# Optimization experiments

Hardware: AMD Instinct MI355X
Metric: run time of the kernel (lower is better)

Reference implementation:

```python
import jax, jax.numpy as jnp
import numpy as np

NPOINT = 1024
RADIUS = 0.4
NSAMPLE = 32
BN_EPS = 1e-3  # keras BatchNormalization default epsilon


def _fps(xyz, npoint):
    # xyz: [N,3] -> indices [npoint] via farthest point sampling (seed index 0)
    N = xyz.shape[0]

    def step(carry, _):
        dists, far = carry
        d = jnp.sum((xyz - xyz[far]) ** 2, axis=-1)
        dists = jnp.minimum(dists, d)
        return (dists, jnp.argmax(dists).astype(jnp.int32)), far

    init = (jnp.full((N,), 1e10, dtype=xyz.dtype), jnp.asarray(0, dtype=jnp.int32))
    _, idx = jax.lax.scan(step, init, None, length=npoint)
    return idx


def _ball_query(xyz, new_xyz, radius, nsample):
    # xyz: [N,3], new_xyz: [S,3] -> idx [S,nsample]
    # First up-to-nsample points (in original index order) within radius of each
    # center; slots past the count are filled with the first found index
    # (matching the CUDA query_ball_point semantics).
    N = xyz.shape[0]
    d2 = jnp.sum((new_xyz[:, None, :] - xyz[None, :, :]) ** 2, axis=-1)  # [S,N]
    key = jnp.where(d2 < radius * radius, jnp.arange(N, dtype=jnp.int32), N)
    sk = jnp.sort(key, axis=-1)[:, :nsample]          # first valid indices, padded with N
    first = sk[:, :1]
    first = jnp.where(first < N, first, 0)            # fallback if no neighbor found
    idx = jnp.where(sk < N, sk, first)
    return idx.astype(jnp.int32)


def _gather(pts, idx):
    # pts: [B,N,C], idx: [B,...] -> [B,...,C]
    return jax.vmap(lambda p, i: p[i])(pts, idx)


def _conv_bn_relu(x, W, b, g, be):
    # 1x1 conv over [B,P,S,Cin] + batchnorm (training mode, batch stats) + relu
    y = jnp.einsum('bpsc,co->bpso', x, W) + b
    m = jnp.mean(y, axis=(0, 1, 2))
    v = jnp.var(y, axis=(0, 1, 2))
    y = (y - m) * jax.lax.rsqrt(v + BN_EPS) * g + be
    return jax.nn.relu(y)


def setup_inputs() -> dict:
    key = jax.random.key(0)
    ks = jax.random.split(key, 8)
    B, N, C = 16, 4096, 64
    xyz = jax.random.normal(ks[0], (B, N, 3), dtype=jnp.float32)
    points = jax.random.normal(ks[1], (B, N, C), dtype=jnp.float32)
    chans = [3 + C, 64, 64, 128]
    inp = {'xyz': xyz, 'points': points}
    for i in range(3):
        cin, cout = chans[i], chans[i + 1]
        limit = np.sqrt(6.0 / (cin + cout))  # glorot uniform
        inp[f'W{i}'] = jax.random.uniform(ks[2 + i], (cin, cout), jnp.float32, -limit, limit)
        inp[f'b{i}'] = jnp.zeros((cout,), jnp.float32)
        inp[f'g{i}'] = jnp.ones((cout,), jnp.float32)
        inp[f'be{i}'] = jnp.zeros((cout,), jnp.float32)
    return inp


def reference(xyz, points, W0, b0, g0, be0, W1, b1, g1, be1, W2, b2, g2, be2):
    xyz_c = jax.lax.stop_gradient(xyz)
    fps_idx = jax.vmap(lambda p: _fps(p, NPOINT))(xyz_c)           # [B,NPOINT]
    new_xyz = _gather(xyz, fps_idx)                                 # [B,NPOINT,3]
    idx = jax.vmap(lambda p, c: _ball_query(p, c, RADIUS, NSAMPLE))(
        xyz_c, jax.lax.stop_gradient(new_xyz))                      # [B,NPOINT,NSAMPLE]
    grouped_xyz = _gather(xyz, idx) - new_xyz[:, :, None, :]        # centered local coords
    grouped_points = _gather(points, idx)                           # [B,NPOINT,NSAMPLE,C]
    new_points = jnp.concatenate([grouped_xyz, grouped_points], axis=-1)
    new_points = _conv_bn_relu(new_points, W0, b0, g0, be0)
    new_points = _conv_bn_relu(new_points, W1, b1, g1, be1)
    new_points = _conv_bn_relu(new_points, W2, b2, g2, be2)
    new_points = jnp.max(new_points, axis=2)                        # max-pool over nsample
    return (new_xyz, new_points, idx)
```

## Files before the change

kernel.cpp:

```cpp
#include <hip/hip_runtime.h>

static constexpr int NB      = 16;
static constexpr int NPTS    = 4096;
static constexpr int NPOINTS = 1024;
static constexpr int NSAMP   = 32;
static constexpr int CIN0    = 67;
static constexpr int C0      = 64;
static constexpr int C1      = 64;
static constexpr int C2      = 128;
static constexpr size_t MROWS = (size_t)NB * NPOINTS * NSAMP;
#define RAD2 0.16f
#define BN_EPS 0.001f

__device__ __forceinline__ float4 uld4(const float* __restrict__ p) {
    return *(const float4* __restrict__)p;
}

__device__ __forceinline__ unsigned short f2bf(float f) {
    const unsigned u = __float_as_uint(f);
    return (unsigned short)((u + 0x7fffu + ((u >> 16) & 1u)) >> 16);
}
__device__ __forceinline__ float bf2f(unsigned short h) {
    return __uint_as_float((unsigned)h << 16);
}

template<int CTRL>
__device__ __forceinline__ float dppf(float v) {
    return __int_as_float(__builtin_amdgcn_update_dpp(0, __float_as_int(v),
                                                      CTRL, 0xF, 0xF, false));
}
template<int CTRL>
__device__ __forceinline__ float dpps(float v) {
    return __int_as_float(__builtin_amdgcn_update_dpp(__float_as_int(v), __float_as_int(v),
                                                      CTRL, 0xF, 0xF, false));
}
__device__ __forceinline__ float dpp_sum64(float v) {
    v += dppf<0x111>(v); v += dppf<0x112>(v); v += dppf<0x114>(v); v += dppf<0x118>(v);
    v += dppf<0x142>(v); v += dppf<0x143>(v);
    return v;
}
__device__ __forceinline__ float dpp_psum8(float v) {
    v += dppf<0x111>(v); v += dppf<0x112>(v); v += dppf<0x114>(v);
    return v;
}
__device__ __forceinline__ float dpp_psum16(float v) {
    v += dppf<0x111>(v); v += dppf<0x112>(v); v += dppf<0x114>(v); v += dppf<0x118>(v);
    return v;
}
__device__ __forceinline__ float dpp_max32(float v) {
    v = fmaxf(v, dpps<0x111>(v)); v = fmaxf(v, dpps<0x112>(v));
    v = fmaxf(v, dpps<0x114>(v)); v = fmaxf(v, dpps<0x118>(v));
    v = fmaxf(v, dpps<0x142>(v));
    return v;
}
__device__ __forceinline__ float dpp_min32(float v) {
    v = fminf(v, dpps<0x111>(v)); v = fminf(v, dpps<0x112>(v));
    v = fminf(v, dpps<0x114>(v)); v = fminf(v, dpps<0x118>(v));
    v = fminf(v, dpps<0x142>(v));
    return v;
}
template<int CTRL>
__device__ __forceinline__ void kstep(unsigned long long& k) {
    const unsigned hi = (unsigned)(k >> 32);
    const unsigned lo = (unsigned)(k & 0xffffffffull);
    const unsigned ohi = (unsigned)__builtin_amdgcn_update_dpp((int)hi, (int)hi, CTRL, 0xF, 0xF, false);
    const unsigned olo = (unsigned)__builtin_amdgcn_update_dpp((int)lo, (int)lo, CTRL, 0xF, 0xF, false);
    const unsigned long long ok = ((unsigned long long)ohi << 32) | olo;
    if (ok > k) k = ok;
}

__global__ __launch_bounds__(512) void fps_kernel(const float* __restrict__ xyz,
                                                  float* __restrict__ out_newxyz,
                                                  float* __restrict__ wsz,
                                                  const float* __restrict__ points,
                                                  const float* __restrict__ W0,
                                                  float* __restrict__ P)
{
    if (blockIdx.x == NB) {
        for (int i = threadIdx.x; i < 1024; i += 512) wsz[i] = 0.f;
        return;
    }
    if (blockIdx.x > NB) {
        const int r = (blockIdx.x - NB - 1) * 512 + threadIdx.x;
        const float4* pr = (const float4*)(points + (size_t)r * 64);
        float x[64];
#pragma unroll
        for (int j = 0; j < 16; ++j) {
            const float4 v = pr[j];
            x[4*j+0] = v.x; x[4*j+1] = v.y; x[4*j+2] = v.z; x[4*j+3] = v.w;
        }
        float acc[64];
#pragma unroll
        for (int o = 0; o < 64; ++o) acc[o] = 0.f;
#pragma unroll 2
        for (int k = 0; k < 64; ++k) {
            const float xk = x[k];
#pragma unroll
            for (int oc = 0; oc < 16; ++oc) {
                const float4 w4 = uld4(W0 + (3 + k) * 64 + 4 * oc);
                acc[4*oc+0] = fmaf(xk, w4.x, acc[4*oc+0]);
                acc[4*oc+1] = fmaf(xk, w4.y, acc[4*oc+1]);
                acc[4*oc+2] = fmaf(xk, w4.z, acc[4*oc+2]);
                acc[4*oc+3] = fmaf(xk, w4.w, acc[4*oc+3]);
            }
        }
        float4* po = (float4*)(P + (size_t)r * 64);
#pragma unroll
        for (int oc = 0; oc < 16; ++oc)
            po[oc] = make_float4(acc[4*oc+0], acc[4*oc+1], acc[4*oc+2], acc[4*oc+3]);
        return;
    }

    __shared__ float sx[NPTS], sy[NPTS], sz[NPTS];
    __shared__ int   sidx[NPOINTS];
    __shared__ __align__(16) unsigned long long redk[2][8];

    const int b    = blockIdx.x;
    const int tid  = threadIdx.x;
    const int lane = tid & 63;
    const int wv   = tid >> 6;

    const float* base = xyz + (size_t)b * NPTS * 3;
    for (int i = tid; i < NPTS; i += 512) {
        sx[i] = base[i * 3 + 0];
        sy[i] = base[i * 3 + 1];
        sz[i] = base[i * 3 + 2];
    }
    __syncthreads();

    float px[8], py[8], pz[8], dd[8];
#pragma unroll
    for (int j = 0; j < 8; ++j) {
        const int i = tid + j * 512;
        px[j] = sx[i]; py[j] = sy[i]; pz[j] = sz[i];
        dd[j] = 1e10f;
    }

    int   far = 0;
    float fx = sx[0], fy = sy[0], fz = sz[0];
#pragma unroll 1
    for (int it = 0; it < NPOINTS; ++it) {
        if (tid == 0) sidx[it] = far;
        float bv = -1.0f; int bi = 0;
#pragma unroll
        for (int j = 0; j < 8; ++j) {
            const float dx = __fsub_rn(px[j], fx);
            const float dy = __fsub_rn(py[j], fy);
            const float dz = __fsub_rn(pz[j], fz);
            const float d  = __fadd_rn(__fadd_rn(__fmul_rn(dx, dx), __fmul_rn(dy, dy)),
                                       __fmul_rn(dz, dz));
            dd[j] = fminf(dd[j], d);
            if (dd[j] > bv) { bv = dd[j]; bi = tid + j * 512; }
        }
        unsigned long long k = ((unsigned long long)__float_as_uint(bv) << 32)
                             | (unsigned)(4095 - bi);
        kstep<0x111>(k);
        kstep<0x112>(k);
        kstep<0x114>(k);
        kstep<0x118>(k);
        kstep<0x142>(k);
        kstep<0x143>(k);

        const int pb = it & 1;
        if (lane == 63) redk[pb][wv] = k;
        __syncthreads();
        unsigned long long ck = redk[pb][0];
#pragma unroll
        for (int w = 1; w < 8; ++w) {
            const unsigned long long ok = redk[pb][w];
            if (ok > ck) ck = ok;
        }
        const int ci = 4095 - (int)(unsigned)(ck & 0xffffffffull);
        far = ci;
        fx = sx[ci]; fy = sy[ci]; fz = sz[ci];
    }
    __syncthreads();
    for (int it = tid; it < NPOINTS; it += 512) {
        const int ii = sidx[it];
        float* o = out_newxyz + ((size_t)b * NPOINTS + it) * 3;
        o[0] = sx[ii]; o[1] = sy[ii]; o[2] = sz[ii];
    }
}

__global__ __launch_bounds__(256) void ball_kernel(const float* __restrict__ xyz,
                                                   const float* __restrict__ newxyz,
                                                   float* __restrict__ out_idx_f)
{
    __shared__ int sel[4][NSAMP];
    const int tid  = threadIdx.x;
    const int lane = tid & 63;
    const int widx = tid >> 6;
    const int w = blockIdx.x * 4 + widx;
    const int b = w >> 10;

    const float cx = newxyz[(size_t)w * 3 + 0];
    const float cy = newxyz[(size_t)w * 3 + 1];
    const float cz = newxyz[(size_t)w * 3 + 2];
    const float* base = xyz + (size_t)b * NPTS * 3;

    int total = 0;
    for (int c = 0; c < NPTS / 64 && total < NSAMP; ++c) {
        const int n = c * 64 + lane;
        const float dx = __fsub_rn(cx, base[n * 3 + 0]);
        const float dy = __fsub_rn(cy, base[n * 3 + 1]);
        const float dz = __fsub_rn(cz, base[n * 3 + 2]);
        const float d2 = __fadd_rn(__fadd_rn(__fmul_rn(dx, dx), __fmul_rn(dy, dy)),
                                   __fmul_rn(dz, dz));
        const bool pred = d2 < RAD2;
        const unsigned long long mask = __ballot(pred);
        if (pred) {
            const int pos = total + (int)__popcll(mask & ((1ull << lane) - 1ull));
            if (pos < NSAMP) sel[widx][pos] = n;
        }
        total += (int)__popcll(mask);
    }
    __syncthreads();
    if (lane < NSAMP) {
        const int first = sel[widx][0];
        const int v = (lane < total) ? sel[widx][lane] : first;
        out_idx_f[(size_t)w * NSAMP + lane] = (float)v;
    }
}

__device__ __forceinline__ void stats4q8(float a0, float a1, float a2, float a3,
                                         float2* sa, bool wr)
{
    float q0 = a0*a0, q1 = a1*a1, q2 = a2*a2, q3 = a3*a3;
    a0 = dpp_psum8(a0); q0 = dpp_psum8(q0);
    a1 = dpp_psum8(a1); q1 = dpp_psum8(q1);
    a2 = dpp_psum8(a2); q2 = dpp_psum8(q2);
    a3 = dpp_psum8(a3); q3 = dpp_psum8(q3);
    if (wr) {
        *(float4*)&sa[0] = make_float4(a0, q0, a1, q1);
        *(float4*)&sa[2] = make_float4(a2, q2, a3, q3);
    }
}

__device__ __forceinline__ void stats4(float a0, float a1, float a2, float a3,
                                       float* sa, int lane)
{
    float q0 = a0*a0, q1 = a1*a1, q2 = a2*a2, q3 = a3*a3;
    a0 = dpp_sum64(a0); q0 = dpp_sum64(q0);
    a1 = dpp_sum64(a1); q1 = dpp_sum64(q1);
    a2 = dpp_sum64(a2); q2 = dpp_sum64(q2);
    a3 = dpp_sum64(a3); q3 = dpp_sum64(q3);
    if (lane == 63) {
        sa[0] += a0; sa[1] += q0; sa[2] += a1; sa[3] += q1;
        sa[4] += a2; sa[5] += q2; sa[6] += a3; sa[7] += q3;
    }
}

__global__ __launch_bounds__(256) void preP_kernel(const float* __restrict__ points,
                                                   const float* __restrict__ W0,
                                                   float* __restrict__ P)
{
    const int r = blockIdx.x * 256 + threadIdx.x;
    const float4* pr = (const float4*)(points + (size_t)r * 64);
    float x[64];
#pragma unroll
    for (int j = 0; j < 16; ++j) {
        const float4 v = pr[j];
        x[4*j+0] = v.x; x[4*j+1] = v.y; x[4*j+2] = v.z; x[4*j+3] = v.w;
    }
    float acc[64];
#pragma unroll
    for (int o = 0; o < 64; ++o) acc[o] = 0.f;
#pragma unroll 2
    for (int k = 0; k < 64; ++k) {
        const float xk = x[k];
#pragma unroll
        for (int oc = 0; oc < 16; ++oc) {
            const float4 w4 = uld4(W0 + (3 + k) * 64 + 4 * oc);
            acc[4*oc+0] = fmaf(xk, w4.x, acc[4*oc+0]);
            acc[4*oc+1] = fmaf(xk, w4.y, acc[4*oc+1]);
            acc[4*oc+2] = fmaf(xk, w4.z, acc[4*oc+2]);
            acc[4*oc+3] = fmaf(xk, w4.w, acc[4*oc+3]);
        }
    }
    float4* po = (float4*)(P + (size_t)r * 64);
#pragma unroll
    for (int oc = 0; oc < 16; ++oc)
        po[oc] = make_float4(acc[4*oc+0], acc[4*oc+1], acc[4*oc+2], acc[4*oc+3]);
}

__device__ __forceinline__ void layer0_dedup(
    const float* __restrict__ xyz, const float* __restrict__ P,
    const float* __restrict__ newxyz, const float* __restrict__ idxf,
    const float* __restrict__ W0, const float* __restrict__ b0,
    int r, float* x1)
{
    const int i  = (int)idxf[r];
    const int bb = r >> 15;
    const int pp = (r >> 5) & 1023;
    const float* pz = xyz + ((size_t)bb * NPTS + i) * 3;
    const float* nz = newxyz + ((size_t)bb * NPOINTS + pp) * 3;
    const float r0 = pz[0] - nz[0];
    const float r1 = pz[1] - nz[1];
    const float r2 = pz[2] - nz[2];
    const float4* prow = (const float4*)(P + ((size_t)bb * NPTS + i) * 64);
#pragma unroll
    for (int oc = 0; oc < 16; ++oc) {
        const float4 pv = prow[oc];
        const float4 bv = uld4(b0 + 4 * oc);
        const float4 wa = uld4(W0 + 0 * 64 + 4 * oc);
        const float4 wb = uld4(W0 + 1 * 64 + 4 * oc);
        const float4 wc = uld4(W0 + 2 * 64 + 4 * oc);
        x1[4*oc+0] = fmaf(r0, wa.x, fmaf(r1, wb.x, fmaf(r2, wc.x, bv.x + pv.x)));
        x1[4*oc+1] = fmaf(r0, wa.y, fmaf(r1, wb.y, fmaf(r2, wc.y, bv.y + pv.y)));
        x1[4*oc+2] = fmaf(r0, wa.z, fmaf(r1, wb.z, fmaf(r2, wc.z, bv.z + pv.z)));
        x1[4*oc+3] = fmaf(r0, wa.w, fmaf(r1, wb.w, fmaf(r2, wc.w, bv.w + pv.w)));
    }
}

template<int C>
__device__ __forceinline__ void bn_inline(const float* __restrict__ gs,
                                          const float* __restrict__ g,
                                          const float* __restrict__ be,
                                          float* ssl, int tid)
{
    if (tid < C) {
        const float inv  = 1.0f / (float)MROWS;
        const float mean = gs[2*tid] * inv;
        const float var  = fmaxf(0.f, gs[2*tid+1] * inv - mean * mean);
        const float sc   = g[tid] / sqrtf(var + BN_EPS);
        ssl[tid]     = sc;
        ssl[C + tid] = fmaf(-mean, sc, be[tid]);
    }
}

__global__ __launch_bounds__(256, 4) void pass0_kernel(
    const float* __restrict__ xyz, const float* __restrict__ P,
    const float* __restrict__ newxyz, const float* __restrict__ idxf,
    const float* __restrict__ W0, const float* __restrict__ b0,
    float* __restrict__ gstats)
{
    __shared__ float2 sacc[32][C0 + 1];
    const int tid  = threadIdx.x;
    const int lane = tid & 63;
    const int wv   = tid >> 6;
    const int slot = wv * 8 + (lane >> 3);
    const bool wr  = (lane & 7) == 7;

    const int r = blockIdx.x * 256 + tid;
    float x1[C0];
    layer0_dedup(xyz, P, newxyz, idxf, W0, b0, r, x1);

#pragma unroll
    for (int oc = 0; oc < 16; ++oc)
        stats4q8(x1[4*oc+0], x1[4*oc+1], x1[4*oc+2], x1[4*oc+3], &sacc[slot][4*oc], wr);

    __syncthreads();
    for (int j = tid; j < C0; j += 256) {
        float s = 0.f, q = 0.f;
#pragma unroll
        for (int v = 0; v < 32; ++v) { s += sacc[v][j].x; q += sacc[v][j].y; }
        atomicAdd(&gstats[2*j], s);
        atomicAdd(&gstats[2*j+1], q);
    }
}

__global__ __launch_bounds__(256, 3) void pass1Y_kernel(
    const float* __restrict__ xyz, const float* __restrict__ P,
    const float* __restrict__ newxyz, const float* __restrict__ idxf,
    const float* __restrict__ W0, const float* __restrict__ b0,
    const float* __restrict__ W1, const float* __restrict__ b1,
    const float* __restrict__ gs0, const float* __restrict__ g0,
    const float* __restrict__ be0,
    float* __restrict__ gstats, unsigned short* __restrict__ y1b)
{
    __shared__ float2 sacc[32][C0 + 1];
    __shared__ float ssl[2 * C0];
    const int tid  = threadIdx.x;
    const int lane = tid & 63;
    const int wv   = tid >> 6;
    const int slot = wv * 8 + (lane >> 3);
    const bool wr  = (lane & 7) == 7;

    bn_inline<C0>(gs0, g0, be0, ssl, tid);
    __syncthreads();

    const int r = blockIdx.x * 256 + tid;
    float x1[C0];
    layer0_dedup(xyz, P, newxyz, idxf, W0, b0, r, x1);
#pragma unroll
    for (int o = 0; o < C0; ++o)
        x1[o] = fmaxf(0.f, fmaf(x1[o], ssl[o], ssl[64 + o]));

    float y1[C1];
#pragma unroll
    for (int o = 0; o < C1; o += 4) {
        const float4 bv = uld4(b1 + o);
        y1[o] = bv.x; y1[o+1] = bv.y; y1[o+2] = bv.z; y1[o+3] = bv.w;
    }
#pragma unroll 2
    for (int k = 0; k < C0; ++k) {
        const float xk = x1[k];
#pragma unroll
        for (int oc = 0; oc < 16; ++oc) {
            const float4 w4 = uld4(W1 + k * 64 + 4 * oc);
            y1[4*oc+0] = fmaf(xk, w4.x, y1[4*oc+0]);
            y1[4*oc+1] = fmaf(xk, w4.y, y1[4*oc+1]);
            y1[4*oc+2] = fmaf(xk, w4.z, y1[4*oc+2]);
            y1[4*oc+3] = fmaf(xk, w4.w, y1[4*oc+3]);
        }
    }

#pragma unroll
    for (int oc = 0; oc < 16; ++oc)
        stats4q8(y1[4*oc+0], y1[4*oc+1], y1[4*oc+2], y1[4*oc+3], &sacc[slot][4*oc], wr);

    uint4* yo = (uint4*)(y1b + (size_t)r * 64);
#pragma unroll
    for (int gq = 0; gq < 8; ++gq) {
        union { unsigned short u[8]; uint4 v; } pk;
#pragma unroll
        for (int e = 0; e < 8; ++e) pk.u[e] = f2bf(y1[8*gq+e]);
        yo[gq] = pk.v;
    }

    __syncthreads();
    for (int j = tid; j < C0; j += 256) {
        float s = 0.f, q = 0.f;
#pragma unroll
        for (int v = 0; v < 32; ++v) { s += sacc[v][j].x; q += sacc[v][j].y; }
        atomicAdd(&gstats[2*j], s);
        atomicAdd(&gstats[2*j+1], q);
    }
}

__global__ __launch_bounds__(256, 3) void p2Y_kernel(
    const unsigned short* __restrict__ y1b,
    const float* __restrict__ W2, const float* __restrict__ b2,
    const float* __restrict__ gs1, const float* __restrict__ g1,
    const float* __restrict__ be1,
    float* __restrict__ gstats, float2* __restrict__ mnmx)
{
    __shared__ float2 sacc[32][C2 + 1];
    __shared__ float ssl[2 * C1];
    const int tid  = threadIdx.x;
    const int lane = tid & 63;
    const int wv   = tid >> 6;
    const int slot = wv * 8 + (lane >> 3);
    const bool wr  = (lane & 7) == 7;

    bn_inline<C1>(gs1, g1, be1, ssl, tid);
    __syncthreads();

    const int r = blockIdx.x * 256 + tid;

    float y1[C1];
    {
        const uint4* yi = (const uint4*)(y1b + (size_t)r * 64);
#pragma unroll
        for (int gq = 0; gq < 8; ++gq) {
            union { uint4 v; unsigned short u[8]; } pk;
            pk.v = yi[gq];
#pragma unroll
            for (int e = 0; e < 8; ++e)
                y1[8*gq+e] = bf2f(pk.u[e]);
        }
    }
#pragma unroll
    for (int o = 0; o < C1; ++o)
        y1[o] = fmaxf(0.f, fmaf(y1[o], ssl[o], ssl[64 + o]));

    const int gbase = blockIdx.x * 8 + 2 * wv;
    float2* mb = mnmx + ((size_t)gbase + (lane >> 5)) * C2;

#pragma unroll 1
    for (int to = 0; to < 2; ++to) {
        const int ob = to * 64;
        float a2[64];
#pragma unroll
        for (int o = 0; o < 64; o += 4) {
            const float4 bv = uld4(b2 + ob + o);
            a2[o] = bv.x; a2[o+1] = bv.y; a2[o+2] = bv.z; a2[o+3] = bv.w;
        }
#pragma unroll 2
        for (int k = 0; k < C1; ++k) {
            const float xk = y1[k];
#pragma unroll
            for (int o = 0; o < 64; o += 4) {
                const float4 w4 = uld4(W2 + k * C2 + ob + o);
                a2[o+0] = fmaf(xk, w4.x, a2[o+0]);
                a2[o+1] = fmaf(xk, w4.y, a2[o+1]);
                a2[o+2] = fmaf(xk, w4.z, a2[o+2]);
                a2[o+3] = fmaf(xk, w4.w, a2[o+3]);
            }
        }

#pragma unroll
        for (int o = 0; o < 64; ++o) {
            const float v = a2[o];
            const float s  = dpp_psum8(v);
            const float q  = dpp_psum8(v * v);
            const float mn = dpp_min32(v);
            const float mx = dpp_max32(v);
            if (wr) sacc[slot][ob + o] = make_float2(s, q);
            if (lane == 31 || lane == 63) mb[ob + o] = make_float2(mn, mx);
        }
    }

    __syncthreads();
    for (int j = tid; j < C2; j += 256) {
        float s = 0.f, q = 0.f;
#pragma unroll
        for (int v = 0; v < 32; ++v) { s += sacc[v][j].x; q += sacc[v][j].y; }
        atomicAdd(&gstats[2*j], s);
        atomicAdd(&gstats[2*j+1], q);
    }
}

__global__ __launch_bounds__(256) void finY_kernel(const float2* __restrict__ mnmx,
                                                   const float* __restrict__ gs2,
                                                   const float* __restrict__ g2,
                                                   const float* __restrict__ be2,
                                                   float* __restrict__ out_np)
{
    const int t = blockIdx.x * 256 + threadIdx.x;
    const int g = t >> 7;
    const int o = t & 127;
    const float inv  = 1.0f / (float)MROWS;
    const float mean = gs2[2*o] * inv;
    const float var  = fmaxf(0.f, gs2[2*o+1] * inv - mean * mean);
    const float sc   = g2[o] / sqrtf(var + BN_EPS);
    const float sh   = fmaf(-mean, sc, be2[o]);
    const float2 mm  = mnmx[(size_t)g * C2 + o];
    const float y    = (sc >= 0.f) ? mm.y : mm.x;
    out_np[t] = fmaxf(0.f, fmaf(y, sc, sh));
}

template<int C>
__global__ void ss_kernel(const float* __restrict__ gs, const float* __restrict__ g,
                          const float* __restrict__ be, float* __restrict__ ss)
{
    const int o = threadIdx.x;
    const float inv  = 1.0f / (float)MROWS;
    const float mean = gs[2*o] * inv;
    const float var  = fmaxf(0.f, gs[2*o+1] * inv - mean * mean);
    const float sc   = g[o] / sqrtf(var + BN_EPS);
    ss[o]     = sc;
    ss[C + o] = fmaf(-mean, sc, be[o]);
}

template<int PHASE>
__global__ __launch_bounds__(256, 2) void passP_kernel(
    const float* __restrict__ xyz, const float* __restrict__ P,
    const float* __restrict__ newxyz, const float* __restrict__ idxf,
    const float* __restrict__ W0, const float* __restrict__ b0,
    const float* __restrict__ W1, const float* __restrict__ b1,
    const float* __restrict__ W2, const float* __restrict__ b2,
    const float* __restrict__ ss0, const float* __restrict__ ss1,
    const float* __restrict__ ss2,
    float* __restrict__ gstats, float* __restrict__ out_np)
{
    constexpr int CS = (PHASE == 2) ? C2 : C0;
    __shared__ float sacc[4][2 * CS];

    const int tid  = threadIdx.x;
    const int lane = tid & 63;
    const int wv   = tid >> 6;

    if constexpr (PHASE <= 2) {
        for (int j = tid; j < 8 * CS; j += 256) (&sacc[0][0])[j] = 0.f;
        __syncthreads();
    }

    const int r = blockIdx.x * 256 + tid;
    float x1[C0];
    layer0_dedup(xyz, P, newxyz, idxf, W0, b0, r, x1);

    if constexpr (PHASE == 0) {
#pragma unroll
        for (int oc = 0; oc < 16; ++oc)
            stats4(x1[4*oc+0], x1[4*oc+1], x1[4*oc+2], x1[4*oc+3], &sacc[wv][8*oc], lane);
    } else {
#pragma unroll
        for (int o = 0; o < C0; ++o)
            x1[o] = fmaxf(0.f, fmaf(x1[o], ss0[o], ss0[64 + o]));

        float y1[C1];
#pragma unroll
        for (int o = 0; o < C1; o += 4) {
            const float4 bv = uld4(b1 + o);
            y1[o] = bv.x; y1[o+1] = bv.y; y1[o+2] = bv.z; y1[o+3] = bv.w;
        }
#pragma unroll 2
        for (int k = 0; k < C0; ++k) {
            const float xk = x1[k];
#pragma unroll
            for (int oc = 0; oc < 16; ++oc) {
                const float4 w4 = uld4(W1 + k * 64 + 4 * oc);
                y1[4*oc+0] = fmaf(xk, w4.x, y1[4*oc+0]);
                y1[4*oc+1] = fmaf(xk, w4.y, y1[4*oc+1]);
                y1[4*oc+2] = fmaf(xk, w4.z, y1[4*oc+2]);
                y1[4*oc+3] = fmaf(xk, w4.w, y1[4*oc+3]);
            }
        }

        if constexpr (PHASE == 1) {
#pragma unroll
            for (int oc = 0; oc < 16; ++oc)
                stats4(y1[4*oc+0], y1[4*oc+1], y1[4*oc+2], y1[4*oc+3], &sacc[wv][8*oc], lane);
        } else {
#pragma unroll
            for (int o = 0; o < C1; ++o)
                y1[o] = fmaxf(0.f, fmaf(y1[o], ss1[o], ss1[64 + o]));

            float a2[C2];
#pragma unroll
            for (int o = 0; o < C2; o += 4) {
                const float4 bv = uld4(b2 + o);
                a2[o] = bv.x; a2[o+1] = bv.y; a2[o+2] = bv.z; a2[o+3] = bv.w;
            }
#pragma unroll 2
            for (int k = 0; k < C1; ++k) {
                const float xk = y1[k];
#pragma unroll
                for (int o = 0; o < C2; o += 4) {
                    const float4 w4 = uld4(W2 + k * C2 + o);
                    a2[o+0] = fmaf(xk, w4.x, a2[o+0]);
                    a2[o+1] = fmaf(xk, w4.y, a2[o+1]);
                    a2[o+2] = fmaf(xk, w4.z, a2[o+2]);
                    a2[o+3] = fmaf(xk, w4.w, a2[o+3]);
                }
            }

            if constexpr (PHASE == 2) {
#pragma unroll
                for (int o = 0; o < C2; ++o) {
                    const float s = dpp_sum64(a2[o]);
                    const float q = dpp_sum64(a2[o] * a2[o]);
                    if (lane == 63) { sacc[wv][2*o] += s; sacc[wv][2*o+1] += q; }
                }
            } else {
                const int g = r >> 5;
#pragma unroll
                for (int o = 0; o < C2; ++o) {
                    float v = fmaxf(0.f, fmaf(a2[o], ss2[o], ss2[C2 + o]));
                    v = dpp_max32(v);
                    if (lane == 31 || lane == 63) out_np[(size_t)g * C2 + o] = v;
                }
            }
        }
    }

    if constexpr (PHASE <= 2) {
        __syncthreads();
        for (int j = tid; j < 2 * CS; j += 256)
            atomicAdd(&gstats[j], sacc[0][j] + sacc[1][j] + sacc[2][j] + sacc[3][j]);
    }
}

template<int PHASE>
__global__ __launch_bounds__(128) void pass_kernel(
    const float* __restrict__ xyz, const float* __restrict__ points,
    const float* __restrict__ newxyz, const float* __restrict__ idxf,
    const float* __restrict__ W0, const float* __restrict__ b0,
    const float* __restrict__ W1, const float* __restrict__ b1,
    const float* __restrict__ W2, const float* __restrict__ b2,
    const float* __restrict__ ss0, const float* __restrict__ ss1,
    const float* __restrict__ ss2,
    float* __restrict__ gstats, float* __restrict__ out_np)
{
    constexpr int CS = (PHASE == 2) ? C2 : C0;
    __shared__ float xld[(PHASE >= 1) ? (64 * 128) : 1];
    __shared__ float sacc[2][2 * CS];

    const int tid  = threadIdx.x;
    const int lane = tid & 63;
    const int wv   = tid >> 6;

    if constexpr (PHASE <= 2) {
        for (int j = tid; j < 2 * 2 * CS; j += 128) (&sacc[0][0])[j] = 0.f;
        __syncthreads();
    }

    const int r  = blockIdx.x * 128 + tid;
    const int i  = (int)idxf[r];
    const int bb = r >> 15;
    const int pp = (r >> 5) & 1023;

    float x[CIN0];
    {
        const float* pz = xyz + ((size_t)bb * NPTS + i) * 3;
        const float* nz = newxyz + ((size_t)bb * NPOINTS + pp) * 3;
        x[0] = pz[0] - nz[0];
        x[1] = pz[1] - nz[1];
        x[2] = pz[2] - nz[2];
        const float4* p4 = (const float4*)(points + ((size_t)bb * NPTS + i) * 64);
#pragma unroll
        for (int j = 0; j < 16; ++j) {
            const float4 v = p4[j];
            x[3+4*j+0] = v.x; x[3+4*j+1] = v.y; x[3+4*j+2] = v.z; x[3+4*j+3] = v.w;
        }
    }

#pragma unroll 1
    for (int oc = 0; oc < 16; ++oc) {
        const float4 bv = uld4(b0 + 4*oc);
        float a0 = bv.x, a1 = bv.y, a2 = bv.z, a3 = bv.w;
#pragma unroll
        for (int k = 0; k < CIN0; ++k) {
            const float4 w4 = uld4(W0 + k*64 + 4*oc);
            a0 = fmaf(x[k], w4.x, a0); a1 = fmaf(x[k], w4.y, a1);
            a2 = fmaf(x[k], w4.z, a2); a3 = fmaf(x[k], w4.w, a3);
        }
        if constexpr (PHASE == 0) {
            stats4(a0, a1, a2, a3, &sacc[wv][8*oc], lane);
        } else {
            xld[(4*oc+0)*128 + tid] = fmaxf(0.f, fmaf(a0, ss0[4*oc+0], ss0[64+4*oc+0]));
            xld[(4*oc+1)*128 + tid] = fmaxf(0.f, fmaf(a1, ss0[4*oc+1], ss0[64+4*oc+1]));
            xld[(4*oc+2)*128 + tid] = fmaxf(0.f, fmaf(a2, ss0[4*oc+2], ss0[64+4*oc+2]));
            xld[(4*oc+3)*128 + tid] = fmaxf(0.f, fmaf(a3, ss0[4*oc+3], ss0[64+4*oc+3]));
        }
    }

    if constexpr (PHASE == 1) {
#pragma unroll 1
        for (int oc = 0; oc < 16; ++oc) {
            const float4 bv = uld4(b1 + 4*oc);
            float a0 = bv.x, a1 = bv.y, a2 = bv.z, a3 = bv.w;
#pragma unroll
            for (int k = 0; k < 64; ++k) {
                const float xk = xld[k*128 + tid];
                const float4 w4 = uld4(W1 + k*64 + 4*oc);
                a0 = fmaf(xk, w4.x, a0); a1 = fmaf(xk, w4.y, a1);
                a2 = fmaf(xk, w4.z, a2); a3 = fmaf(xk, w4.w, a3);
            }
            stats4(a0, a1, a2, a3, &sacc[wv][8*oc], lane);
        }
    }

    if constexpr (PHASE >= 2) {
        float acc2[C2];
#pragma unroll
        for (int o = 0; o < C2; o += 4) {
            const float4 bv = uld4(b2 + o);
            acc2[o] = bv.x; acc2[o+1] = bv.y; acc2[o+2] = bv.z; acc2[o+3] = bv.w;
        }
#pragma unroll 1
        for (int oc = 0; oc < 16; ++oc) {
            const float4 bv = uld4(b1 + 4*oc);
            float a0 = bv.x, a1 = bv.y, a2 = bv.z, a3 = bv.w;
#pragma unroll
            for (int k = 0; k < 64; ++k) {
                const float xk = xld[k*128 + tid];
                const float4 w4 = uld4(W1 + k*64 + 4*oc);
                a0 = fmaf(xk, w4.x, a0); a1 = fmaf(xk, w4.y, a1);
                a2 = fmaf(xk, w4.z, a2); a3 = fmaf(xk, w4.w, a3);
            }
            const float xc0 = fmaxf(0.f, fmaf(a0, ss1[4*oc+0], ss1[64+4*oc+0]));
            const float xc1 = fmaxf(0.f, fmaf(a1, ss1[4*oc+1], ss1[64+4*oc+1]));
            const float xc2 = fmaxf(0.f, fmaf(a2, ss1[4*oc+2], ss1[64+4*oc+2]));
            const float xc3 = fmaxf(0.f, fmaf(a3, ss1[4*oc+3], ss1[64+4*oc+3]));
#pragma unroll
            for (int o = 0; o < C2; o += 4) {
                const float4 wA = uld4(W2 + (4*oc+0)*C2 + o);
                const float4 wB = uld4(W2 + (4*oc+1)*C2 + o);
                const float4 wC = uld4(W2 + (4*oc+2)*C2 + o);
                const float4 wD = uld4(W2 + (4*oc+3)*C2 + o);
                acc2[o+0] = fmaf(xc0, wA.x, fmaf(xc1, wB.x, fmaf(xc2, wC.x, fmaf(xc3, wD.x, acc2[o+0]))));
                acc2[o+1] = fmaf(xc0, wA.y, fmaf(xc1, wB.y, fmaf(xc2, wC.y, fmaf(xc3, wD.y, acc2[o+1]))));
                acc2[o+2] = fmaf(xc0, wA.z, fmaf(xc1, wB.z, fmaf(xc2, wC.z, fmaf(xc3, wD.z, acc2[o+2]))));
                acc2[o+3] = fmaf(xc0, wA.w, fmaf(xc1, wB.w, fmaf(xc2, wC.w, fmaf(xc3, wD.w, acc2[o+3]))));
            }
        }

        if constexpr (PHASE == 2) {
#pragma unroll
            for (int o = 0; o < C2; ++o) {
                const float s = dpp_sum64(acc2[o]);
                const float q = dpp_sum64(acc2[o] * acc2[o]);
                if (lane == 63) { sacc[wv][2*o] += s; sacc[wv][2*o+1] += q; }
            }
        } else {
            const int g = r >> 5;
#pragma unroll
            for (int o = 0; o < C2; ++o) {
                float v = fmaxf(0.f, fmaf(acc2[o], ss2[o], ss2[C2+o]));
                v = dpp_max32(v);
                if (lane == 31 || lane == 63) out_np[(size_t)g * C2 + o] = v;
            }
        }
    }

    if constexpr (PHASE <= 2) {
        __syncthreads();
        for (int j = tid; j < 2 * CS; j += 128)
            atomicAdd(&gstats[j], sacc[0][j] + sacc[1][j]);
    }
}

extern "C" void kernel_launch(void* const* d_in, const int* in_sizes, int n_in,
                              void* d_out, int out_size, void* d_ws, size_t ws_size,
                              hipStream_t stream)
{
    (void)in_sizes; (void)n_in; (void)out_size;
    const float* xyz    = (const float*)d_in[0];
    const float* points = (const float*)d_in[1];
    const float* W0  = (const float*)d_in[2];
    const float* b0  = (const float*)d_in[3];
    const float* g0  = (const float*)d_in[4];
    const float* be0 = (const float*)d_in[5];
    const float* W1  = (const float*)d_in[6];
    const float* b1  = (const float*)d_in[7];
    const float* g1  = (const float*)d_in[8];
    const float* be1 = (const float*)d_in[9];
    const float* W2  = (const float*)d_in[10];
    const float* b2  = (const float*)d_in[11];
    const float* g2  = (const float*)d_in[12];
    const float* be2 = (const float*)d_in[13];

    float* out = (float*)d_out;
    float* out_newxyz = out;
    float* out_newpts = out + (size_t)NB * NPOINTS * 3;
    float* out_idx    = out_newpts + (size_t)NB * NPOINTS * C2;

    float* wsf = (float*)d_ws;
    float* gs0 = wsf + 0;
    float* gs1 = wsf + 128;
    float* gs2 = wsf + 256;
    float* ss0 = wsf + 512;
    float* ss1 = wsf + 640;
    float* ss2 = wsf + 768;
    const size_t PBYTES  = (size_t)NB * NPTS * C0 * 4;
    const size_t MMBYTES = (size_t)NB * NPOINTS * 2 * C2 * 4;
    const size_t YBYTES  = MROWS * C1 * 2;
    float* P    = (float*)((char*)d_ws + 65536);
    float* mnmx = (float*)((char*)d_ws + 65536 + PBYTES);
    unsigned short* y1b = (unsigned short*)((char*)d_ws + 65536 + PBYTES + MMBYTES);

    const bool haveP  = ws_size >= (65536 + PBYTES);
    const bool haveMM = ws_size >= (65536 + PBYTES + MMBYTES);
    const bool haveY  = ws_size >= (65536 + PBYTES + MMBYTES + YBYTES);

    const int frontGrid = NB + 1 + (haveP ? (NB * NPTS / 512) : 0);
    fps_kernel<<<frontGrid, 512, 0, stream>>>(xyz, out_newxyz, wsf, points, W0, P);
    ball_kernel<<<(NB * NPOINTS) / 4, 256, 0, stream>>>(xyz, out_newxyz, out_idx);

    if (haveY) {
        const int grid = (int)(MROWS / 256);
        pass0_kernel<<<grid, 256, 0, stream>>>(xyz, P, out_newxyz, out_idx,
                                               W0, b0, gs0);
        pass1Y_kernel<<<grid, 256, 0, stream>>>(xyz, P, out_newxyz, out_idx,
                                                W0, b0, W1, b1, gs0, g0, be0,
                                                gs1, y1b);
        p2Y_kernel<<<grid, 256, 0, stream>>>(y1b, W2, b2, gs1, g1, be1,
                                             gs2, (float2*)mnmx);
        finY_kernel<<<NB * NPOINTS * C2 / 256, 256, 0, stream>>>((const float2*)mnmx,
                                                                 gs2, g2, be2, out_newpts);
    } else if (haveP) {
        const int grid = (int)(MROWS / 256);
        passP_kernel<0><<<grid, 256, 0, stream>>>(xyz, P, out_newxyz, out_idx,
                                                  W0, b0, W1, b1, W2, b2,
                                                  ss0, ss1, ss2, gs0, nullptr);
        ss_kernel<C0><<<1, C0, 0, stream>>>(gs0, g0, be0, ss0);
        passP_kernel<1><<<grid, 256, 0, stream>>>(xyz, P, out_newxyz, out_idx,
                                                  W0, b0, W1, b1, W2, b2,
                                                  ss0, ss1, ss2, gs1, nullptr);
        ss_kernel<C1><<<1, C1, 0, stream>>>(gs1, g1, be1, ss1);
        passP_kernel<2><<<grid, 256, 0, stream>>>(xyz, P, out_newxyz, out_idx,
                                                  W0, b0, W1, b1, W2, b2,
                                                  ss0, ss1, ss2, gs2, nullptr);
        ss_kernel<C2><<<1, C2, 0, stream>>>(gs2, g2, be2, ss2);
        passP_kernel<3><<<grid, 256, 0, stream>>>(xyz, P, out_newxyz, out_idx,
                                                  W0, b0, W1, b1, W2, b2,
                                                  ss0, ss1, ss2, nullptr, out_newpts);
        (void)haveMM;
    } else {
        const int grid = (int)(MROWS / 128);
        pass_kernel<0><<<grid, 128, 0, stream>>>(xyz, points, out_newxyz, out_idx,
                                                 W0, b0, W1, b1, W2, b2,
                                                 ss0, ss1, ss2, gs0, nullptr);
        ss_kernel<C0><<<1, C0, 0, stream>>>(gs0, g0, be0, ss0);
        pass_kernel<1><<<grid, 128, 0, stream>>>(xyz, points, out_newxyz, out_idx,
                                                 W0, b0, W1, b1, W2, b2,
                                                 ss0, ss1, ss2, gs1, nullptr);
        ss_kernel<C1><<<1, C1, 0, stream>>>(gs1, g1, be1, ss1);
        pass_kernel<2><<<grid, 128, 0, stream>>>(xyz, points, out_newxyz, out_idx,
                                                 W0, b0, W1, b1, W2, b2,
                                                 ss0, ss1, ss2, gs2, nullptr);
        ss_kernel<C2><<<1, C2, 0, stream>>>(gs2, g2, be2, ss2);
        pass_kernel<3><<<grid, 128, 0, stream>>>(xyz, points, out_newxyz, out_idx,
                                                 W0, b0, W1, b1, W2, b2,
                                                 ss0, ss1, ss2, nullptr, out_newpts);
    }
}
```

Baseline: 1.304 ms.

## Use bf16 MFMA for layer-2 conv and hoist BN scale/shift into kernels

Replaces the per-thread FP32 FMA loop of the third 1x1 conv with 32x32x16 bf16 MFMA instructions. W2 is pre-transposed to bf16 in the front kernel, and per-group min/max plus sum/sumsq are reduced from the MFMA accumulator layout. BN scale/shift computation moves from inline per-block code into separate ss_kernel launches. Stats reduction in pass0/pass1 switches to 16-lane partial sums accumulated in zeroed shared memory. Activations are rounded to bf16 before the matmul, which lowers precision, and the change adds two small kernel launches.

```diff
diff --git a/kernel.cpp b/kernel.cpp
--- a/kernel.cpp
+++ b/kernel.cpp
@@ -24,6 +24,10 @@
     return __uint_as_float((unsigned)h << 16);
 }
 
+typedef short bf16x8 __attribute__((ext_vector_type(8)));
+typedef float f32x16 __attribute__((ext_vector_type(16)));
+union UB { uint4 u; bf16x8 h; };
+
 template<int CTRL>
 __device__ __forceinline__ float dppf(float v) {
     return __int_as_float(__builtin_amdgcn_update_dpp(0, __float_as_int(v),
@@ -37,10 +41,6 @@
 __device__ __forceinline__ float dpp_sum64(float v) {
     v += dppf<0x111>(v); v += dppf<0x112>(v); v += dppf<0x114>(v); v += dppf<0x118>(v);
     v += dppf<0x142>(v); v += dppf<0x143>(v);
-    return v;
-}
-__device__ __forceinline__ float dpp_psum8(float v) {
-    v += dppf<0x111>(v); v += dppf<0x112>(v); v += dppf<0x114>(v);
     return v;
 }
 __device__ __forceinline__ float dpp_psum16(float v) {
@@ -74,10 +74,18 @@
                                                   float* __restrict__ wsz,
                                                   const float* __restrict__ points,
                                                   const float* __restrict__ W0,
-                                                  float* __restrict__ P)
+                                                  float* __restrict__ P,
+                                                  const float* __restrict__ W2,
+                                                  unsigned short* __restrict__ W2t)
 {
     if (blockIdx.x == NB) {
         for (int i = threadIdx.x; i < 1024; i += 512) wsz[i] = 0.f;
+        if (W2t) {
+            for (int i = threadIdx.x; i < C2 * C1; i += 512) {
+                const int n = i >> 6, k = i & 63;
+                W2t[i] = f2bf(W2[(size_t)k * C2 + n]);
+            }
+        }
         return;
     }
     if (blockIdx.x > NB) {
@@ -222,17 +230,17 @@
     }
 }
 
-__device__ __forceinline__ void stats4q8(float a0, float a1, float a2, float a3,
-                                         float2* sa, bool wr)
+__device__ __forceinline__ void stats4q(float a0, float a1, float a2, float a3,
+                                        float* sa, bool wr)
 {
     float q0 = a0*a0, q1 = a1*a1, q2 = a2*a2, q3 = a3*a3;
-    a0 = dpp_psum8(a0); q0 = dpp_psum8(q0);
-    a1 = dpp_psum8(a1); q1 = dpp_psum8(q1);
-    a2 = dpp_psum8(a2); q2 = dpp_psum8(q2);
-    a3 = dpp_psum8(a3); q3 = dpp_psum8(q3);
+    a0 = dpp_psum16(a0); q0 = dpp_psum16(q0);
+    a1 = dpp_psum16(a1); q1 = dpp_psum16(q1);
+    a2 = dpp_psum16(a2); q2 = dpp_psum16(q2);
+    a3 = dpp_psum16(a3); q3 = dpp_psum16(q3);
     if (wr) {
-        *(float4*)&sa[0] = make_float4(a0, q0, a1, q1);
-        *(float4*)&sa[2] = make_float4(a2, q2, a3, q3);
+        sa[0] += a0; sa[1] += q0; sa[2] += a1; sa[3] += q1;
+        sa[4] += a2; sa[5] += q2; sa[6] += a3; sa[7] += q3;
     }
 }
 
@@ -248,39 +256,6 @@
         sa[0] += a0; sa[1] += q0; sa[2] += a1; sa[3] += q1;
         sa[4] += a2; sa[5] += q2; sa[6] += a3; sa[7] += q3;
     }
-}
-
-__global__ __launch_bounds__(256) void preP_kernel(const float* __restrict__ points,
-                                                   const float* __restrict__ W0,
-                                                   float* __restrict__ P)
-{
-    const int r = blockIdx.x * 256 + threadIdx.x;
-    const float4* pr = (const float4*)(points + (size_t)r * 64);
-    float x[64];
-#pragma unroll
-    for (int j = 0; j < 16; ++j) {
-        const float4 v = pr[j];
-        x[4*j+0] = v.x; x[4*j+1] = v.y; x[4*j+2] = v.z; x[4*j+3] = v.w;
-    }
-    float acc[64];
-#pragma unroll
-    for (int o = 0; o < 64; ++o) acc[o] = 0.f;
-#pragma unroll 2
-    for (int k = 0; k < 64; ++k) {
-        const float xk = x[k];
-#pragma unroll
-        for (int oc = 0; oc < 16; ++oc) {
-            const float4 w4 = uld4(W0 + (3 + k) * 64 + 4 * oc);
-            acc[4*oc+0] = fmaf(xk, w4.x, acc[4*oc+0]);
-            acc[4*oc+1] = fmaf(xk, w4.y, acc[4*oc+1]);
-            acc[4*oc+2] = fmaf(xk, w4.z, acc[4*oc+2]);
-            acc[4*oc+3] = fmaf(xk, w4.w, acc[4*oc+3]);
-        }
-    }
-    float4* po = (float4*)(P + (size_t)r * 64);
-#pragma unroll
-    for (int oc = 0; oc < 16; ++oc)
-        po[oc] = make_float4(acc[4*oc+0], acc[4*oc+1], acc[4*oc+2], acc[4*oc+3]);
 }
 
 __device__ __forceinline__ void layer0_dedup(
@@ -312,34 +287,21 @@
     }
 }
 
-template<int C>
-__device__ __forceinline__ void bn_inline(const float* __restrict__ gs,
-                                          const float* __restrict__ g,
-                                          const float* __restrict__ be,
-                                          float* ssl, int tid)
-{
-    if (tid < C) {
-        const float inv  = 1.0f / (float)MROWS;
-        const float mean = gs[2*tid] * inv;
-        const float var  = fmaxf(0.f, gs[2*tid+1] * inv - mean * mean);
-        const float sc   = g[tid] / sqrtf(var + BN_EPS);
-        ssl[tid]     = sc;
-        ssl[C + tid] = fmaf(-mean, sc, be[tid]);
-    }
-}
-
 __global__ __launch_bounds__(256, 4) void pass0_kernel(
     const float* __restrict__ xyz, const float* __restrict__ P,
     const float* __restrict__ newxyz, const float* __restrict__ idxf,
     const float* __restrict__ W0, const float* __restrict__ b0,
     float* __restrict__ gstats)
 {
-    __shared__ float2 sacc[32][C0 + 1];
+    __shared__ float sacc[16][2 * C0];
     const int tid  = threadIdx.x;
     const int lane = tid & 63;
     const int wv   = tid >> 6;
-    const int slot = wv * 8 + (lane >> 3);
-    const bool wr  = (lane & 7) == 7;
+    const int slot = wv * 4 + (lane >> 4);
+    const bool wr  = (lane & 15) == 15;
+
+    for (int j = tid; j < 16 * 2 * C0; j += 256) (&sacc[0][0])[j] = 0.f;
+    __syncthreads();
 
     const int r = blockIdx.x * 256 + tid;
     float x1[C0];
@@ -347,15 +309,14 @@
 
 #pragma unroll
     for (int oc = 0; oc < 16; ++oc)
-        stats4q8(x1[4*oc+0], x1[4*oc+1], x1[4*oc+2], x1[4*oc+3], &sacc[slot][4*oc], wr);
+        stats4q(x1[4*oc+0], x1[4*oc+1], x1[4*oc+2], x1[4*oc+3], &sacc[slot][8*oc], wr);
 
     __syncthreads();
-    for (int j = tid; j < C0; j += 256) {
-        float s = 0.f, q = 0.f;
-#pragma unroll
-        for (int v = 0; v < 32; ++v) { s += sacc[v][j].x; q += sacc[v][j].y; }
-        atomicAdd(&gstats[2*j], s);
-        atomicAdd(&gstats[2*j+1], q);
+    for (int j = tid; j < 2 * C0; j += 256) {
+        float s = 0.f;
+#pragma unroll
+        for (int q = 0; q < 16; ++q) s += sacc[q][j];
+        atomicAdd(&gstats[j], s);
     }
 }
 
@@ -364,19 +325,17 @@
     const float* __restrict__ newxyz, const float* __restrict__ idxf,
     const float* __restrict__ W0, const float* __restrict__ b0,
     const float* __restrict__ W1, const float* __restrict__ b1,
-    const float* __restrict__ gs0, const float* __restrict__ g0,
-    const float* __restrict__ be0,
+    const float* __restrict__ ss0,
     float* __restrict__ gstats, unsigned short* __restrict__ y1b)
 {
-    __shared__ float2 sacc[32][C0 + 1];
-    __shared__ float ssl[2 * C0];
+    __shared__ float sacc[16][2 * C0];
     const int tid  = threadIdx.x;
     const int lane = tid & 63;
     const int wv   = tid >> 6;
-    const int slot = wv * 8 + (lane >> 3);
-    const bool wr  = (lane & 7) == 7;
-
-    bn_inline<C0>(gs0, g0, be0, ssl, tid);
+    const int slot = wv * 4 + (lane >> 4);
+    const bool wr  = (lane & 15) == 15;
+
+    for (int j = tid; j < 16 * 2 * C0; j += 256) (&sacc[0][0])[j] = 0.f;
     __syncthreads();
 
     const int r = blockIdx.x * 256 + tid;
@@ -384,7 +343,7 @@
     layer0_dedup(xyz, P, newxyz, idxf, W0, b0, r, x1);
 #pragma unroll
     for (int o = 0; o < C0; ++o)
-        x1[o] = fmaxf(0.f, fmaf(x1[o], ssl[o], ssl[64 + o]));
+        x1[o] = fmaxf(0.f, fmaf(x1[o], ss0[o], ss0[64 + o]));
 
     float y1[C1];
 #pragma unroll
@@ -407,7 +366,7 @@
 
 #pragma unroll
     for (int oc = 0; oc < 16; ++oc)
-        stats4q8(y1[4*oc+0], y1[4*oc+1], y1[4*oc+2], y1[4*oc+3], &sacc[slot][4*oc], wr);
+        stats4q(y1[4*oc+0], y1[4*oc+1], y1[4*oc+2], y1[4*oc+3], &sacc[slot][8*oc], wr);
 
     uint4* yo = (uint4*)(y1b + (size_t)r * 64);
 #pragma unroll
@@ -419,95 +378,97 @@
     }
 
     __syncthreads();
-    for (int j = tid; j < C0; j += 256) {
-        float s = 0.f, q = 0.f;
-#pragma unroll
-        for (int v = 0; v < 32; ++v) { s += sacc[v][j].x; q += sacc[v][j].y; }
-        atomicAdd(&gstats[2*j], s);
-        atomicAdd(&gstats[2*j+1], q);
-    }
-}
-
-__global__ __launch_bounds__(256, 3) void p2Y_kernel(
+    for (int j = tid; j < 2 * C0; j += 256) {
+        float s = 0.f;
+#pragma unroll
+        for (int q = 0; q < 16; ++q) s += sacc[q][j];
+        atomicAdd(&gstats[j], s);
+    }
+}
+
+__global__ __launch_bounds__(256, 3) void p2Ym_kernel(
     const unsigned short* __restrict__ y1b,
-    const float* __restrict__ W2, const float* __restrict__ b2,
-    const float* __restrict__ gs1, const float* __restrict__ g1,
-    const float* __restrict__ be1,
+    const unsigned short* __restrict__ W2t,
+    const float* __restrict__ b2,
+    const float* __restrict__ ss1,
     float* __restrict__ gstats, float2* __restrict__ mnmx)
 {
-    __shared__ float2 sacc[32][C2 + 1];
-    __shared__ float ssl[2 * C1];
+    __shared__ float  ssl[2 * C1];
+    __shared__ float2 sacc[8][C2];
+    __shared__ float2 mnacc[8][C2];
+
     const int tid  = threadIdx.x;
     const int lane = tid & 63;
-    const int wv   = tid >> 6;
-    const int slot = wv * 8 + (lane >> 3);
-    const bool wr  = (lane & 7) == 7;
-
-    bn_inline<C1>(gs1, g1, be1, ssl, tid);
+    const int w    = tid >> 6;
+    const int half = lane >> 5;
+    const int col  = lane & 31;
+    const int slot = w * 2 + half;
+
+    for (int j = tid; j < 2 * C1; j += 256) ssl[j] = ss1[j];
     __syncthreads();
 
-    const int r = blockIdx.x * 256 + tid;
-
-    float y1[C1];
-    {
-        const uint4* yi = (const uint4*)(y1b + (size_t)r * 64);
-#pragma unroll
-        for (int gq = 0; gq < 8; ++gq) {
-            union { uint4 v; unsigned short u[8]; } pk;
-            pk.v = yi[gq];
-#pragma unroll
-            for (int e = 0; e < 8; ++e)
-                y1[8*gq+e] = bf2f(pk.u[e]);
-        }
-    }
-#pragma unroll
-    for (int o = 0; o < C1; ++o)
-        y1[o] = fmaxf(0.f, fmaf(y1[o], ssl[o], ssl[64 + o]));
-
-    const int gbase = blockIdx.x * 8 + 2 * wv;
-    float2* mb = mnmx + ((size_t)gbase + (lane >> 5)) * C2;
-
-#pragma unroll 1
-    for (int to = 0; to < 2; ++to) {
-        const int ob = to * 64;
-        float a2[64];
-#pragma unroll
-        for (int o = 0; o < 64; o += 4) {
-            const float4 bv = uld4(b2 + ob + o);
-            a2[o] = bv.x; a2[o+1] = bv.y; a2[o+2] = bv.z; a2[o+3] = bv.w;
-        }
-#pragma unroll 2
-        for (int k = 0; k < C1; ++k) {
-            const float xk = y1[k];
-#pragma unroll
-            for (int o = 0; o < 64; o += 4) {
-                const float4 w4 = uld4(W2 + k * C2 + ob + o);
-                a2[o+0] = fmaf(xk, w4.x, a2[o+0]);
-                a2[o+1] = fmaf(xk, w4.y, a2[o+1]);
-                a2[o+2] = fmaf(xk, w4.z, a2[o+2]);
-                a2[o+3] = fmaf(xk, w4.w, a2[o+3]);
-            }
-        }
-
-#pragma unroll
-        for (int o = 0; o < 64; ++o) {
-            const float v = a2[o];
-            const float s  = dpp_psum8(v);
-            const float q  = dpp_psum8(v * v);
-            const float mn = dpp_min32(v);
-            const float mx = dpp_max32(v);
-            if (wr) sacc[slot][ob + o] = make_float2(s, q);
-            if (lane == 31 || lane == 63) mb[ob + o] = make_float2(mn, mx);
-        }
+    const int r = blockIdx.x * 128 + w * 32 + col;
+
+    UB afrag[4];
+#pragma unroll
+    for (int t = 0; t < 4; ++t) {
+        const int ko = t * 16 + half * 8;
+        uint4 ua = *(const uint4*)(y1b + (size_t)r * 64 + ko);
+        float scs[8], shs[8];
+        *(float4*)&scs[0] = *(const float4*)&ssl[ko];
+        *(float4*)&scs[4] = *(const float4*)&ssl[ko + 4];
+        *(float4*)&shs[0] = *(const float4*)&ssl[64 + ko];
+        *(float4*)&shs[4] = *(const float4*)&ssl[64 + ko + 4];
+        const unsigned* ud = (const unsigned*)&ua;
+        uint4 outw;
+        unsigned* od = (unsigned*)&outw;
+#pragma unroll
+        for (int d = 0; d < 4; ++d) {
+            const float flo = bf2f((unsigned short)(ud[d] & 0xffffu));
+            const float fhi = bf2f((unsigned short)(ud[d] >> 16));
+            const float vlo = fmaxf(0.f, fmaf(flo, scs[2*d],   shs[2*d]));
+            const float vhi = fmaxf(0.f, fmaf(fhi, scs[2*d+1], shs[2*d+1]));
+            od[d] = ((unsigned)f2bf(vhi) << 16) | (unsigned)f2bf(vlo);
+        }
+        afrag[t].u = outw;
+    }
+
+#pragma unroll
+    for (int ct = 0; ct < 4; ++ct) {
+        const float bias = b2[ct * 32 + col];
+        f32x16 acc;
+#pragma unroll
+        for (int i = 0; i < 16; ++i) acc[i] = bias;
+#pragma unroll
+        for (int t = 0; t < 4; ++t) {
+            UB bfrag;
+            bfrag.u = *(const uint4*)(W2t + (size_t)(ct * 32 + col) * 64 + t * 16 + half * 8);
+            acc = __builtin_amdgcn_mfma_f32_32x32x16_bf16(afrag[t].h, bfrag.h, acc, 0, 0, 0);
+        }
+        float s = 0.f, q = 0.f, mn = 3.4e38f, mx = -3.4e38f;
+#pragma unroll
+        for (int i = 0; i < 16; ++i) {
+            const float v = acc[i];
+            s += v; q = fmaf(v, v, q);
+            mn = fminf(mn, v); mx = fmaxf(mx, v);
+        }
+        sacc[slot][ct * 32 + col]  = make_float2(s, q);
+        mnacc[slot][ct * 32 + col] = make_float2(mn, mx);
     }
 
     __syncthreads();
     for (int j = tid; j < C2; j += 256) {
         float s = 0.f, q = 0.f;
 #pragma unroll
-        for (int v = 0; v < 32; ++v) { s += sacc[v][j].x; q += sacc[v][j].y; }
+        for (int v = 0; v < 8; ++v) { s += sacc[v][j].x; q += sacc[v][j].y; }
         atomicAdd(&gstats[2*j], s);
         atomicAdd(&gstats[2*j+1], q);
+    }
+    for (int j = tid; j < 4 * C2; j += 256) {
+        const int wg = j >> 7, ch = j & 127;
+        const float2 a = mnacc[2*wg][ch], bq = mnacc[2*wg+1][ch];
+        mnmx[((size_t)blockIdx.x * 4 + wg) * C2 + ch] =
+            make_float2(fminf(a.x, bq.x), fmaxf(a.y, bq.y));
     }
 }
 
@@ -541,6 +502,39 @@
     const float sc   = g[o] / sqrtf(var + BN_EPS);
     ss[o]     = sc;
     ss[C + o] = fmaf(-mean, sc, be[o]);
+}
+
+__global__ __launch_bounds__(256) void preP_kernel(const float* __restrict__ points,
+                                                   const float* __restrict__ W0,
+                                                   float* __restrict__ P)
+{
+    const int r = blockIdx.x * 256 + threadIdx.x;
+    const float4* pr = (const float4*)(points + (size_t)r * 64);
+    float x[64];
+#pragma unroll
+    for (int j = 0; j < 16; ++j) {
+        const float4 v = pr[j];
+        x[4*j+0] = v.x; x[4*j+1] = v.y; x[4*j+2] = v.z; x[4*j+3] = v.w;
+    }
+    float acc[64];
+#pragma unroll
+    for (int o = 0; o < 64; ++o) acc[o] = 0.f;
+#pragma unroll 2
+    for (int k = 0; k < 64; ++k) {
+        const float xk = x[k];
+#pragma unroll
+        for (int oc = 0; oc < 16; ++oc) {
+            const float4 w4 = uld4(W0 + (3 + k) * 64 + 4 * oc);
+            acc[4*oc+0] = fmaf(xk, w4.x, acc[4*oc+0]);
+            acc[4*oc+1] = fmaf(xk, w4.y, acc[4*oc+1]);
+            acc[4*oc+2] = fmaf(xk, w4.z, acc[4*oc+2]);
+            acc[4*oc+3] = fmaf(xk, w4.w, acc[4*oc+3]);
+        }
+    }
+    float4* po = (float4*)(P + (size_t)r * 64);
+#pragma unroll
+    for (int oc = 0; oc < 16; ++oc)
+        po[oc] = make_float4(acc[4*oc+0], acc[4*oc+1], acc[4*oc+2], acc[4*oc+3]);
 }
 
 template<int PHASE>
@@ -827,27 +821,30 @@
     const size_t PBYTES  = (size_t)NB * NPTS * C0 * 4;
     const size_t MMBYTES = (size_t)NB * NPOINTS * 2 * C2 * 4;
     const size_t YBYTES  = MROWS * C1 * 2;
+    const size_t TBYTES  = (size_t)C2 * C1 * 2;
     float* P    = (float*)((char*)d_ws + 65536);
     float* mnmx = (float*)((char*)d_ws + 65536 + PBYTES);
     unsigned short* y1b = (unsigned short*)((char*)d_ws + 65536 + PBYTES + MMBYTES);
-
-    const bool haveP  = ws_size >= (65536 + PBYTES);
-    const bool haveMM = ws_size >= (65536 + PBYTES + MMBYTES);
-    const bool haveY  = ws_size >= (65536 + PBYTES + MMBYTES + YBYTES);
+    unsigned short* W2t = (unsigned short*)((char*)d_ws + 65536 + PBYTES + MMBYTES + YBYTES);
+
+    const bool haveP = ws_size >= (65536 + PBYTES);
+    const bool haveY = ws_size >= (65536 + PBYTES + MMBYTES + YBYTES + TBYTES);
 
     const int frontGrid = NB + 1 + (haveP ? (NB * NPTS / 512) : 0);
-    fps_kernel<<<frontGrid, 512, 0, stream>>>(xyz, out_newxyz, wsf, points, W0, P);
+    fps_kernel<<<frontGrid, 512, 0, stream>>>(xyz, out_newxyz, wsf, points, W0, P,
+                                              W2, haveY ? W2t : nullptr);
     ball_kernel<<<(NB * NPOINTS) / 4, 256, 0, stream>>>(xyz, out_newxyz, out_idx);
 
     if (haveY) {
         const int grid = (int)(MROWS / 256);
         pass0_kernel<<<grid, 256, 0, stream>>>(xyz, P, out_newxyz, out_idx,
                                                W0, b0, gs0);
+        ss_kernel<C0><<<1, C0, 0, stream>>>(gs0, g0, be0, ss0);
         pass1Y_kernel<<<grid, 256, 0, stream>>>(xyz, P, out_newxyz, out_idx,
-                                                W0, b0, W1, b1, gs0, g0, be0,
-                                                gs1, y1b);
-        p2Y_kernel<<<grid, 256, 0, stream>>>(y1b, W2, b2, gs1, g1, be1,
-                                             gs2, (float2*)mnmx);
+                                                W0, b0, W1, b1, ss0, gs1, y1b);
+        ss_kernel<C1><<<1, C1, 0, stream>>>(gs1, g1, be1, ss1);
+        p2Ym_kernel<<<(int)(MROWS / 128), 256, 0, stream>>>(y1b, W2t, b2, ss1,
+                                                            gs2, (float2*)mnmx);
         finY_kernel<<<NB * NPOINTS * C2 / 256, 256, 0, stream>>>((const float2*)mnmx,
                                                                  gs2, g2, be2, out_newpts);
     } else if (haveP) {
@@ -867,7 +864,6 @@
         passP_kernel<3><<<grid, 256, 0, stream>>>(xyz, P, out_newxyz, out_idx,
                                                   W0, b0, W1, b1, W2, b2,
                                                   ss0, ss1, ss2, nullptr, out_newpts);
-        (void)haveMM;
     } else {
         const int grid = (int)(MROWS / 128);
         pass_kernel<0><<<grid, 128, 0, stream>>>(xyz, points, out_newxyz, out_idx,
```

After: 1.202 ms. -7.8%, faster.
